# Performance work log

Measured on AMD Instinct MI355X. Metric: run time of the kernel, lower is better.

Reference implementation:

```python
import jax, jax.numpy as jnp
import numpy as np

E, TOPK, H, F, CAP, TP = 8, 2, 1024, 4096, 2048, 1
N = 8192  # tokens * topk (token copies)


def setup_inputs() -> dict:
    key = jax.random.key(0)
    ks = jax.random.split(key, 6)
    inputs_shard = jax.random.normal(ks[0], (N, H), jnp.float32)
    gate_weight = jax.random.uniform(ks[1], (N,), jnp.float32)
    choosed_experts = jax.random.randint(ks[2], (N,), 0, E, dtype=jnp.int32)
    new_index = jax.random.permutation(ks[3], N).astype(jnp.int32)
    w1 = jax.random.normal(ks[4], (E, F, H), jnp.float32) * 0.02
    w2 = jax.random.normal(ks[5], (E, H, F), jnp.float32) * 0.02
    return {"inputs_shard": inputs_shard, "gate_weight": gate_weight,
            "choosed_experts": choosed_experts, "new_index": new_index,
            "w1": w1, "w2": w2}


def _grouped_expert_mlp(x, experts, w1, w2):
    # capacity-based grouped GEMM: sort token copies by expert, pack into
    # (E, CAP, H), run batched fc1->gelu->fc2, unpack back to token order.
    n = x.shape[0]
    order = jnp.argsort(experts)                      # [N]
    se = experts[order]
    offsets = jnp.searchsorted(se, jnp.arange(E))     # start of each expert block
    rank = jnp.arange(n) - offsets[se]                # within-expert position
    valid = rank < CAP                                # CAP=2*N/E, ~never drops
    slot = jnp.where(valid, se * CAP + rank, E * CAP) # out-of-range -> dropped
    buf = jnp.zeros((E * CAP, x.shape[1]), x.dtype).at[slot].set(x[order], mode="drop")
    xe = buf.reshape(E, CAP, -1)                      # [E, CAP, H]
    h = jax.nn.gelu(jnp.einsum("ech,efh->ecf", xe, w1), approximate=False)
    ye = jnp.einsum("ecf,ehf->ech", h, w2).reshape(E * CAP, -1)
    y_sorted = jnp.where(valid[:, None], ye[jnp.clip(slot, 0, E * CAP - 1)], 0.0)
    return jnp.zeros_like(x).at[order].set(y_sorted)  # back to token-copy order


def reference(inputs_shard, gate_weight, choosed_experts, new_index, w1, w2):
    # expert compute, scaled by router probabilities (combine-side scaling)
    result = _grouped_expert_mlp(inputs_shard, choosed_experts, w1, w2)
    result = result * gate_weight[:, None]
    # scatter combine: output1[new_index] = result; full_output += output1
    full_output = jnp.zeros((N, H), result.dtype).at[new_index].set(result)
    # topk reduce: view(N//topk, topk, H).sum(1)
    topk_reduce = full_output.reshape(N // TOPK, TOPK, H).sum(1)
    # reduce_scatter over TP group; TP=1 => identity
    return topk_reduce
```

## Files before the change

kernel.cpp:

```cpp
#include <hip/hip_runtime.h>
#include <stdint.h>

#define N_TOK 8192
#define HDIM  1024
#define FDIM  4096
#define NEXP  8
#define MAXTILES 72

typedef __attribute__((ext_vector_type(8))) __bf16 bf16x8;
typedef __attribute__((ext_vector_type(8))) unsigned short ushort8v;
typedef __attribute__((ext_vector_type(4))) unsigned short ushort4v;
typedef __attribute__((ext_vector_type(4))) float floatx4;

__device__ __forceinline__ unsigned short f2bf(float f) {
  union { float f; uint32_t u; } v; v.f = f;
  uint32_t u = v.u;
  return (unsigned short)((u + 0x7FFFu + ((u >> 16) & 1u)) >> 16);
}

__device__ __forceinline__ void load_lds16(const void* g, void* l) {
  __builtin_amdgcn_global_load_lds(
      (const __attribute__((address_space(1))) void*)(uintptr_t)g,
      (__attribute__((address_space(3))) void*)(uint32_t)(uintptr_t)l,
      16, 0, 0);
}


__global__ void k_count(const int* __restrict__ experts, int* __restrict__ meta) {
  int i = blockIdx.x * 256 + threadIdx.x;
  atomicAdd(&meta[experts[i]], 1);
}

__global__ void k_plan(int* __restrict__ meta) {
  if (threadIdx.x == 0) {
    int off = 0, nt = 0;
    for (int e = 0; e < NEXP; ++e) {
      int c = meta[e];
      meta[8 + e] = off;
      meta[16 + e] = off;
      int t = (c + 127) >> 7;
      for (int k = 0; k < t; ++k) meta[32 + nt++] = (e << 16) | k;
      off += c;
    }
    meta[24] = nt;
  }
}

__global__ void k_scatter(const int* __restrict__ experts, int* __restrict__ meta,
                          int* __restrict__ order) {
  int i = blockIdx.x * 256 + threadIdx.x;
  int e = experts[i];
  int pos = atomicAdd(&meta[16 + e], 1);
  order[pos] = i;
}

__global__ void k_pack(const float* __restrict__ x, const int* __restrict__ order,
                       unsigned short* __restrict__ xs) {
  int s = blockIdx.x;
  int i = order[s];
  int t = threadIdx.x;
  float4 v = *(const float4*)(x + (size_t)i * HDIM + t * 4);
  ushort4v u;
  u[0] = f2bf(v.x); u[1] = f2bf(v.y); u[2] = f2bf(v.z); u[3] = f2bf(v.w);
  *(ushort4v*)(xs + (size_t)s * HDIM + t * 4) = u;
}

__global__ void k_cvt(const float* __restrict__ src, unsigned short* __restrict__ dst) {
  size_t i = ((size_t)blockIdx.x * 256 + threadIdx.x) * 4;
  float4 v = *(const float4*)(src + i);
  ushort4v u;
  u[0] = f2bf(v.x); u[1] = f2bf(v.y); u[2] = f2bf(v.z); u[3] = f2bf(v.w);
  *(ushort4v*)(dst + i) = u;
}

template <bool PRE>
__global__ __launch_bounds__(256) void gemm1_t(
    const unsigned short* __restrict__ xs, const void* __restrict__ w1v,
    unsigned short* __restrict__ h1, const int* __restrict__ meta) {
  __shared__ unsigned short As[128 * 32];
  __shared__ unsigned short Bs[128 * 32];

  int bx = blockIdx.z;
  if (bx >= meta[24]) return;
  int entry = meta[32 + bx];
  int e = entry >> 16, mt = entry & 0xffff;
  int row0 = meta[8 + e] + mt * 128;
  int rend = meta[8 + e] + meta[e];
  int fBase = blockIdx.x * 128;

  int tid = threadIdx.x;
  int w = tid >> 6, lane = tid & 63;
  int r = lane & 15, q = lane >> 4;
  int wm = (w >> 1) * 64, wn = (w & 1) * 64;

  int ar0 = (w * 16) + (lane >> 2);
  int s0 = min(row0 + ar0, N_TOK - 1);
  int s1 = min(row0 + 64 + ar0, N_TOK - 1);
  const unsigned short* ag0 = xs + (size_t)s0 * HDIM + (lane & 3) * 8;
  const unsigned short* ag1 = xs + (size_t)s1 * HDIM + (lane & 3) * 8;
  unsigned short* al0 = &As[(w * 16) * 32];
  unsigned short* al1 = &As[(64 + w * 16) * 32];

  const unsigned short* bg0 = nullptr; const unsigned short* bg1 = nullptr;
  unsigned short* bl0 = nullptr; unsigned short* bl1 = nullptr;
  const float* wbase = nullptr; int brow = 0, bkk = 0;
  if constexpr (PRE) {
    const unsigned short* wb = (const unsigned short*)w1v;
    int br = w * 16 + (lane >> 2);
    bg0 = wb + ((size_t)e * FDIM + fBase + br) * HDIM + (lane & 3) * 8;
    bg1 = bg0 + (size_t)64 * HDIM;
    bl0 = &Bs[(w * 16) * 32];
    bl1 = &Bs[(64 + w * 16) * 32];
  } else {
    brow = tid >> 1; bkk = (tid & 1) * 16;
    wbase = (const float*)w1v + ((size_t)e * FDIM + fBase + brow) * HDIM + bkk;
  }

  floatx4 acc[4][4];
#pragma unroll
  for (int i = 0; i < 4; ++i)
#pragma unroll
    for (int j = 0; j < 4; ++j) acc[i][j] = (floatx4){0.f, 0.f, 0.f, 0.f};

  for (int k0 = 0; k0 < HDIM; k0 += 32) {
    __syncthreads();
    load_lds16(ag0 + k0, al0);
    load_lds16(ag1 + k0, al1);
    if constexpr (PRE) {
      load_lds16(bg0 + k0, bl0);
      load_lds16(bg1 + k0, bl1);
    } else {
      const float* gb = wbase + k0;
      float4 f0 = *(const float4*)(gb);
      float4 f1 = *(const float4*)(gb + 4);
      float4 f2 = *(const float4*)(gb + 8);
      float4 f3 = *(const float4*)(gb + 12);
      ushort8v u0, u1;
      u0[0] = f2bf(f0.x); u0[1] = f2bf(f0.y); u0[2] = f2bf(f0.z); u0[3] = f2bf(f0.w);
      u0[4] = f2bf(f1.x); u0[5] = f2bf(f1.y); u0[6] = f2bf(f1.z); u0[7] = f2bf(f1.w);
      u1[0] = f2bf(f2.x); u1[1] = f2bf(f2.y); u1[2] = f2bf(f2.z); u1[3] = f2bf(f2.w);
      u1[4] = f2bf(f3.x); u1[5] = f2bf(f3.y); u1[6] = f2bf(f3.z); u1[7] = f2bf(f3.w);
      *(ushort8v*)&Bs[brow * 32 + bkk] = u0;
      *(ushort8v*)&Bs[brow * 32 + bkk + 8] = u1;
    }
    __syncthreads();

    bf16x8 av[4], bv[4];
#pragma unroll
    for (int i = 0; i < 4; ++i)
      av[i] = __builtin_bit_cast(bf16x8, *(const ushort8v*)&As[(wm + i * 16 + r) * 32 + q * 8]);
#pragma unroll
    for (int j = 0; j < 4; ++j)
      bv[j] = __builtin_bit_cast(bf16x8, *(const ushort8v*)&Bs[(wn + j * 16 + r) * 32 + q * 8]);
#pragma unroll
    for (int i = 0; i < 4; ++i)
#pragma unroll
      for (int j = 0; j < 4; ++j)
        acc[i][j] = __builtin_amdgcn_mfma_f32_16x16x32_bf16(av[i], bv[j], acc[i][j], 0, 0, 0);
  }

#pragma unroll
  for (int i = 0; i < 4; ++i) {
    int mrow = row0 + wm + i * 16 + q * 4;
#pragma unroll
    for (int reg = 0; reg < 4; ++reg) {
      int s = mrow + reg;
      if (s < rend) {
        unsigned short* dst = h1 + (size_t)s * FDIM + fBase + wn + r;
#pragma unroll
        for (int j = 0; j < 4; ++j) {
          float v = acc[i][j][reg];
          float g = 0.5f * v * (1.0f + erff(v * 0.70710678118654752f));
          dst[j * 16] = f2bf(g);
        }
      }
    }
  }
}

template <bool PRE>
__global__ __launch_bounds__(256) void gemm2_t(
    const unsigned short* __restrict__ h1, const void* __restrict__ w2v,
    const float* __restrict__ gate, const int* __restrict__ new_index,
    float* __restrict__ out, const int* __restrict__ meta) {
  __shared__ unsigned short As[128 * 32];
  __shared__ unsigned short Bs[128 * 32];

  int bx = blockIdx.z;
  if (bx >= meta[24]) return;
  int entry = meta[32 + bx];
  int e = entry >> 16, mt = entry & 0xffff;
  int row0 = meta[8 + e] + mt * 128;
  int rend = meta[8 + e] + meta[e];
  int nBase = blockIdx.x * 128;
  int kStart = blockIdx.y * (FDIM / 2);
  int kEnd = kStart + (FDIM / 2);
  const int* order = meta + 256;

  int tid = threadIdx.x;
  int w = tid >> 6, lane = tid & 63;
  int r = lane & 15, q = lane >> 4;
  int wm = (w >> 1) * 64, wn = (w & 1) * 64;

  int ar0 = (w * 16) + (lane >> 2);
  int s0 = min(row0 + ar0, N_TOK - 1);
  int s1 = min(row0 + 64 + ar0, N_TOK - 1);
  const unsigned short* ag0 = h1 + (size_t)s0 * FDIM + (lane & 3) * 8;
  const unsigned short* ag1 = h1 + (size_t)s1 * FDIM + (lane & 3) * 8;
  unsigned short* al0 = &As[(w * 16) * 32];
  unsigned short* al1 = &As[(64 + w * 16) * 32];

  const unsigned short* bg0 = nullptr; const unsigned short* bg1 = nullptr;
  unsigned short* bl0 = nullptr; unsigned short* bl1 = nullptr;
  const float* wbase = nullptr; int brow = 0, bkk = 0;
  if constexpr (PRE) {
    const unsigned short* wb = (const unsigned short*)w2v;
    int br = w * 16 + (lane >> 2);
    bg0 = wb + ((size_t)e * HDIM + nBase + br) * FDIM + (lane & 3) * 8;
    bg1 = bg0 + (size_t)64 * FDIM;
    bl0 = &Bs[(w * 16) * 32];
    bl1 = &Bs[(64 + w * 16) * 32];
  } else {
    brow = tid >> 1; bkk = (tid & 1) * 16;
    wbase = (const float*)w2v + ((size_t)e * HDIM + nBase + brow) * FDIM + bkk;
  }

  floatx4 acc[4][4];
#pragma unroll
  for (int i = 0; i < 4; ++i)
#pragma unroll
    for (int j = 0; j < 4; ++j) acc[i][j] = (floatx4){0.f, 0.f, 0.f, 0.f};

  for (int k0 = kStart; k0 < kEnd; k0 += 32) {
    __syncthreads();
    load_lds16(ag0 + k0, al0);
    load_lds16(ag1 + k0, al1);
    if constexpr (PRE) {
      load_lds16(bg0 + k0, bl0);
      load_lds16(bg1 + k0, bl1);
    } else {
      const float* gb = wbase + k0;
      float4 f0 = *(const float4*)(gb);
      float4 f1 = *(const float4*)(gb + 4);
      float4 f2 = *(const float4*)(gb + 8);
      float4 f3 = *(const float4*)(gb + 12);
      ushort8v u0, u1;
      u0[0] = f2bf(f0.x); u0[1] = f2bf(f0.y); u0[2] = f2bf(f0.z); u0[3] = f2bf(f0.w);
      u0[4] = f2bf(f1.x); u0[5] = f2bf(f1.y); u0[6] = f2bf(f1.z); u0[7] = f2bf(f1.w);
      u1[0] = f2bf(f2.x); u1[1] = f2bf(f2.y); u1[2] = f2bf(f2.z); u1[3] = f2bf(f2.w);
      u1[4] = f2bf(f3.x); u1[5] = f2bf(f3.y); u1[6] = f2bf(f3.z); u1[7] = f2bf(f3.w);
      *(ushort8v*)&Bs[brow * 32 + bkk] = u0;
      *(ushort8v*)&Bs[brow * 32 + bkk + 8] = u1;
    }
    __syncthreads();

    bf16x8 av[4], bv[4];
#pragma unroll
    for (int i = 0; i < 4; ++i)
      av[i] = __builtin_bit_cast(bf16x8, *(const ushort8v*)&As[(wm + i * 16 + r) * 32 + q * 8]);
#pragma unroll
    for (int j = 0; j < 4; ++j)
      bv[j] = __builtin_bit_cast(bf16x8, *(const ushort8v*)&Bs[(wn + j * 16 + r) * 32 + q * 8]);
#pragma unroll
    for (int i = 0; i < 4; ++i)
#pragma unroll
      for (int j = 0; j < 4; ++j)
        acc[i][j] = __builtin_amdgcn_mfma_f32_16x16x32_bf16(av[i], bv[j], acc[i][j], 0, 0, 0);
  }

#pragma unroll
  for (int i = 0; i < 4; ++i) {
    int mrow = row0 + wm + i * 16 + q * 4;
#pragma unroll
    for (int reg = 0; reg < 4; ++reg) {
      int s = mrow + reg;
      if (s < rend) {
        int itok = order[s];
        float gw = gate[itok];
        int jdx = new_index[itok];
        float* dst = out + (size_t)(jdx >> 1) * HDIM + nBase + wn + r;
#pragma unroll
        for (int j = 0; j < 4; ++j) atomicAdd(dst + j * 16, acc[i][j][reg] * gw);
      }
    }
  }
}

extern "C" void kernel_launch(void* const* d_in, const int* in_sizes, int n_in,
                              void* d_out, int out_size, void* d_ws, size_t ws_size,
                              hipStream_t stream) {
  const float* x        = (const float*)d_in[0];
  const float* gate     = (const float*)d_in[1];
  const int* experts    = (const int*)d_in[2];
  const int* new_index  = (const int*)d_in[3];
  const float* w1       = (const float*)d_in[4];
  const float* w2       = (const float*)d_in[5];
  float* out            = (float*)d_out;

  int* meta = (int*)d_ws;
  int* order = meta + 256;
  const size_t XS_OFF = 65536;
  const size_t XS_SZ  = (size_t)N_TOK * HDIM * 2;
  const size_t H1_SZ  = (size_t)N_TOK * FDIM * 2;
  const size_t W_SZ   = (size_t)NEXP * FDIM * HDIM * 2;
  unsigned short* xs  = (unsigned short*)((char*)d_ws + XS_OFF);
  unsigned short* h1  = (unsigned short*)((char*)d_ws + XS_OFF + XS_SZ);
  unsigned short* w1b = (unsigned short*)((char*)d_ws + XS_OFF + XS_SZ + H1_SZ);
  unsigned short* w2b = (unsigned short*)((char*)d_ws + XS_OFF + XS_SZ + H1_SZ + W_SZ);
  size_t need_small = XS_OFF + XS_SZ + H1_SZ;
  size_t need_big   = need_small + 2 * W_SZ;
  if (ws_size < need_small) return;
  bool big = ws_size >= need_big;

  hipMemsetAsync(d_ws, 0, 4096, stream);
  hipMemsetAsync(d_out, 0, (size_t)out_size * sizeof(float), stream);
  k_count<<<N_TOK / 256, 256, 0, stream>>>(experts, meta);
  k_plan<<<1, 64, 0, stream>>>(meta);
  k_scatter<<<N_TOK / 256, 256, 0, stream>>>(experts, meta, order);
  k_pack<<<N_TOK, 256, 0, stream>>>(x, order, xs);

  if (big) {
    int nblk = (int)((size_t)NEXP * FDIM * HDIM / 4 / 256);
    k_cvt<<<nblk, 256, 0, stream>>>(w1, w1b);
    k_cvt<<<nblk, 256, 0, stream>>>(w2, w2b);
    gemm1_t<true><<<dim3(FDIM / 128, 1, MAXTILES), 256, 0, stream>>>(xs, w1b, h1, meta);
    gemm2_t<true><<<dim3(HDIM / 128, 2, MAXTILES), 256, 0, stream>>>(h1, w2b, gate, new_index, out, meta);
  } else {
    gemm1_t<false><<<dim3(FDIM / 128, 1, MAXTILES), 256, 0, stream>>>(xs, w1, h1, meta);
    gemm2_t<false><<<dim3(HDIM / 128, 2, MAXTILES), 256, 0, stream>>>(h1, w2, gate, new_index, out, meta);
  }
}
```

Measured before the change: 674.7 us.

## Add 256-row tiled double-buffered GEMM kernels with swizzled LDS for bf16 path

Replaces the pre-converted bf16 GEMM path with new 512-thread kernels that use 256x256 (fc1) and 256x128 (fc2) tiles and a K-step of 64. Loads are double-buffered into LDS with explicit vmcnt waits, and the LDS layout is XOR-swizzled to avoid bank conflicts. MFMA issue runs at raised priority. The planner now also emits a 256-row tile list. The larger tiles aim at more operand reuse and overlap of loads with compute, at the cost of higher register/LDS use, occupancy of one block per CU, and more padded rows per expert tile.

```diff
diff --git a/kernel.cpp b/kernel.cpp
--- a/kernel.cpp
+++ b/kernel.cpp
@@ -6,6 +6,7 @@
 #define FDIM  4096
 #define NEXP  8
 #define MAXTILES 72
+#define MAXT256  40
 
 typedef __attribute__((ext_vector_type(8))) __bf16 bf16x8;
 typedef __attribute__((ext_vector_type(8))) unsigned short ushort8v;
@@ -33,16 +34,19 @@
 
 __global__ void k_plan(int* __restrict__ meta) {
   if (threadIdx.x == 0) {
-    int off = 0, nt = 0;
+    int off = 0, nt = 0, nt2 = 0;
     for (int e = 0; e < NEXP; ++e) {
       int c = meta[e];
       meta[8 + e] = off;
       meta[16 + e] = off;
       int t = (c + 127) >> 7;
       for (int k = 0; k < t; ++k) meta[32 + nt++] = (e << 16) | k;
+      int t2 = (c + 255) >> 8;
+      for (int k = 0; k < t2; ++k) meta[104 + nt2++] = (e << 16) | k;
       off += c;
     }
     meta[24] = nt;
+    meta[25] = nt2;
   }
 }
 
@@ -73,6 +77,231 @@
   *(ushort4v*)(dst + i) = u;
 }
 
+
+#define VM_WAIT(n) asm volatile("s_waitcnt vmcnt(" #n ")" ::: "memory")
+
+__global__ __launch_bounds__(512, 1) void gemm1_big(
+    const unsigned short* __restrict__ xs, const unsigned short* __restrict__ wb,
+    unsigned short* __restrict__ h1, const int* __restrict__ meta) {
+  __shared__ unsigned short As[2][256 * 64];
+  __shared__ unsigned short Bs[2][256 * 64];
+
+  int bx = blockIdx.z;
+  if (bx >= meta[25]) return;
+  int entry = meta[104 + bx];
+  int e = entry >> 16, mt = entry & 0xffff;
+  int row0 = meta[8 + e] + mt * 256;
+  int rend = meta[8 + e] + meta[e];
+  int fBase = blockIdx.x * 256;
+
+  int tid = threadIdx.x;
+  int w = tid >> 6, l = tid & 63;
+  int r = l & 15, q = l >> 4;
+
+  int srow = w * 8 + (l >> 3);
+  int scol = ((l & 7) ^ (l >> 3)) << 3;
+  const unsigned short* aP[4];
+  const unsigned short* bP[4];
+#pragma unroll
+  for (int n = 0; n < 4; ++n) {
+    int ar = min(row0 + n * 64 + srow, N_TOK - 1);
+    aP[n] = xs + (size_t)ar * HDIM + scol;
+    int br = fBase + n * 64 + srow;
+    bP[n] = wb + ((size_t)e * FDIM + br) * HDIM + scol;
+  }
+
+  floatx4 acc[8][4];
+#pragma unroll
+  for (int i = 0; i < 8; ++i)
+#pragma unroll
+    for (int j = 0; j < 4; ++j) acc[i][j] = (floatx4){0.f, 0.f, 0.f, 0.f};
+
+  int mb = (w >> 2) * 128;
+  int nb = (w & 3) * 64;
+
+  {
+#pragma unroll
+    for (int n = 0; n < 4; ++n) load_lds16(aP[n], &As[0][n * 4096 + w * 512]);
+#pragma unroll
+    for (int n = 0; n < 4; ++n) load_lds16(bP[n], &Bs[0][n * 4096 + w * 512]);
+  }
+
+  const int NT = HDIM / 64;
+  for (int kt = 0; kt < NT; ++kt) {
+    int cur = kt & 1;
+    if (kt + 1 < NT) {
+      int ko = (kt + 1) * 64;
+      int nxt = cur ^ 1;
+#pragma unroll
+      for (int n = 0; n < 4; ++n) load_lds16(aP[n] + ko, &As[nxt][n * 4096 + w * 512]);
+#pragma unroll
+      for (int n = 0; n < 4; ++n) load_lds16(bP[n] + ko, &Bs[nxt][n * 4096 + w * 512]);
+      VM_WAIT(8);
+    } else {
+      VM_WAIT(0);
+    }
+    __builtin_amdgcn_s_barrier();
+    __builtin_amdgcn_sched_barrier(0);
+
+#pragma unroll
+    for (int kk = 0; kk < 2; ++kk) {
+      bf16x8 av[8], bv[4];
+#pragma unroll
+      for (int i = 0; i < 8; ++i) {
+        int row = mb + i * 16 + r;
+        int col = (kk * 32 + q * 8) ^ ((r & 7) << 3);
+        av[i] = __builtin_bit_cast(bf16x8, *(const ushort8v*)&As[cur][row * 64 + col]);
+      }
+#pragma unroll
+      for (int j = 0; j < 4; ++j) {
+        int row = nb + j * 16 + r;
+        int col = (kk * 32 + q * 8) ^ ((r & 7) << 3);
+        bv[j] = __builtin_bit_cast(bf16x8, *(const ushort8v*)&Bs[cur][row * 64 + col]);
+      }
+      __builtin_amdgcn_s_setprio(1);
+#pragma unroll
+      for (int i = 0; i < 8; ++i)
+#pragma unroll
+        for (int j = 0; j < 4; ++j)
+          acc[i][j] = __builtin_amdgcn_mfma_f32_16x16x32_bf16(av[i], bv[j], acc[i][j], 0, 0, 0);
+      __builtin_amdgcn_s_setprio(0);
+    }
+    __builtin_amdgcn_s_barrier();
+  }
+
+#pragma unroll
+  for (int i = 0; i < 8; ++i) {
+    int mrow = row0 + mb + i * 16 + q * 4;
+#pragma unroll
+    for (int reg = 0; reg < 4; ++reg) {
+      int s = mrow + reg;
+      if (s < rend) {
+        unsigned short* dst = h1 + (size_t)s * FDIM + fBase + nb + r;
+#pragma unroll
+        for (int j = 0; j < 4; ++j) {
+          float v = acc[i][j][reg];
+          float g = 0.5f * v * (1.0f + erff(v * 0.70710678118654752f));
+          dst[j * 16] = f2bf(g);
+        }
+      }
+    }
+  }
+}
+
+__global__ __launch_bounds__(512, 1) void gemm2_big(
+    const unsigned short* __restrict__ h1, const unsigned short* __restrict__ wb,
+    const float* __restrict__ gate, const int* __restrict__ new_index,
+    float* __restrict__ out, const int* __restrict__ meta) {
+  __shared__ unsigned short As[2][256 * 64];
+  __shared__ unsigned short Bs[2][128 * 64];
+
+  int bx = blockIdx.z;
+  if (bx >= meta[25]) return;
+  int entry = meta[104 + bx];
+  int e = entry >> 16, mt = entry & 0xffff;
+  int row0 = meta[8 + e] + mt * 256;
+  int rend = meta[8 + e] + meta[e];
+  int nBase = blockIdx.x * 128;
+  int kStart = blockIdx.y * (FDIM / 2);
+  const int* order = meta + 256;
+
+  int tid = threadIdx.x;
+  int w = tid >> 6, l = tid & 63;
+  int r = l & 15, q = l >> 4;
+
+  int srow = w * 8 + (l >> 3);
+  int scol = ((l & 7) ^ (l >> 3)) << 3;
+  const unsigned short* aP[4];
+  const unsigned short* bP[2];
+#pragma unroll
+  for (int n = 0; n < 4; ++n) {
+    int ar = min(row0 + n * 64 + srow, N_TOK - 1);
+    aP[n] = h1 + (size_t)ar * FDIM + kStart + scol;
+  }
+#pragma unroll
+  for (int n = 0; n < 2; ++n) {
+    int br = nBase + n * 64 + srow;
+    bP[n] = wb + ((size_t)e * HDIM + br) * FDIM + kStart + scol;
+  }
+
+  floatx4 acc[4][4];
+#pragma unroll
+  for (int i = 0; i < 4; ++i)
+#pragma unroll
+    for (int j = 0; j < 4; ++j) acc[i][j] = (floatx4){0.f, 0.f, 0.f, 0.f};
+
+  int mb = (w >> 1) * 64;
+  int nb = (w & 1) * 64;
+
+  {
+#pragma unroll
+    for (int n = 0; n < 4; ++n) load_lds16(aP[n], &As[0][n * 4096 + w * 512]);
+#pragma unroll
+    for (int n = 0; n < 2; ++n) load_lds16(bP[n], &Bs[0][n * 4096 + w * 512]);
+  }
+
+  const int NT = (FDIM / 2) / 64;
+  for (int kt = 0; kt < NT; ++kt) {
+    int cur = kt & 1;
+    if (kt + 1 < NT) {
+      int ko = (kt + 1) * 64;
+      int nxt = cur ^ 1;
+#pragma unroll
+      for (int n = 0; n < 4; ++n) load_lds16(aP[n] + ko, &As[nxt][n * 4096 + w * 512]);
+#pragma unroll
+      for (int n = 0; n < 2; ++n) load_lds16(bP[n] + ko, &Bs[nxt][n * 4096 + w * 512]);
+      VM_WAIT(6);
+    } else {
+      VM_WAIT(0);
+    }
+    __builtin_amdgcn_s_barrier();
+    __builtin_amdgcn_sched_barrier(0);
+
+#pragma unroll
+    for (int kk = 0; kk < 2; ++kk) {
+      bf16x8 av[4], bv[4];
+#pragma unroll
+      for (int i = 0; i < 4; ++i) {
+        int row = mb + i * 16 + r;
+        int col = (kk * 32 + q * 8) ^ ((r & 7) << 3);
+        av[i] = __builtin_bit_cast(bf16x8, *(const ushort8v*)&As[cur][row * 64 + col]);
+      }
+#pragma unroll
+      for (int j = 0; j < 4; ++j) {
+        int row = nb + j * 16 + r;
+        int col = (kk * 32 + q * 8) ^ ((r & 7) << 3);
+        bv[j] = __builtin_bit_cast(bf16x8, *(const ushort8v*)&Bs[cur][row * 64 + col]);
+      }
+      __builtin_amdgcn_s_setprio(1);
+#pragma unroll
+      for (int i = 0; i < 4; ++i)
+#pragma unroll
+        for (int j = 0; j < 4; ++j)
+          acc[i][j] = __builtin_amdgcn_mfma_f32_16x16x32_bf16(av[i], bv[j], acc[i][j], 0, 0, 0);
+      __builtin_amdgcn_s_setprio(0);
+    }
+    __builtin_amdgcn_s_barrier();
+  }
+
+#pragma unroll
+  for (int i = 0; i < 4; ++i) {
+    int mrow = row0 + mb + i * 16 + q * 4;
+#pragma unroll
+    for (int reg = 0; reg < 4; ++reg) {
+      int s = mrow + reg;
+      if (s < rend) {
+        int itok = order[s];
+        float gw = gate[itok];
+        int jdx = new_index[itok];
+        float* dst = out + (size_t)(jdx >> 1) * HDIM + nBase + nb + r;
+#pragma unroll
+        for (int j = 0; j < 4; ++j) atomicAdd(dst + j * 16, acc[i][j][reg] * gw);
+      }
+    }
+  }
+}
+
+
 template <bool PRE>
 __global__ __launch_bounds__(256) void gemm1_t(
     const unsigned short* __restrict__ xs, const void* __restrict__ w1v,
@@ -101,20 +330,9 @@
   unsigned short* al0 = &As[(w * 16) * 32];
   unsigned short* al1 = &As[(64 + w * 16) * 32];
 
-  const unsigned short* bg0 = nullptr; const unsigned short* bg1 = nullptr;
-  unsigned short* bl0 = nullptr; unsigned short* bl1 = nullptr;
   const float* wbase = nullptr; int brow = 0, bkk = 0;
-  if constexpr (PRE) {
-    const unsigned short* wb = (const unsigned short*)w1v;
-    int br = w * 16 + (lane >> 2);
-    bg0 = wb + ((size_t)e * FDIM + fBase + br) * HDIM + (lane & 3) * 8;
-    bg1 = bg0 + (size_t)64 * HDIM;
-    bl0 = &Bs[(w * 16) * 32];
-    bl1 = &Bs[(64 + w * 16) * 32];
-  } else {
-    brow = tid >> 1; bkk = (tid & 1) * 16;
-    wbase = (const float*)w1v + ((size_t)e * FDIM + fBase + brow) * HDIM + bkk;
-  }
+  brow = tid >> 1; bkk = (tid & 1) * 16;
+  wbase = (const float*)w1v + ((size_t)e * FDIM + fBase + brow) * HDIM + bkk;
 
   floatx4 acc[4][4];
 #pragma unroll
@@ -126,10 +344,7 @@
     __syncthreads();
     load_lds16(ag0 + k0, al0);
     load_lds16(ag1 + k0, al1);
-    if constexpr (PRE) {
-      load_lds16(bg0 + k0, bl0);
-      load_lds16(bg1 + k0, bl1);
-    } else {
+    {
       const float* gb = wbase + k0;
       float4 f0 = *(const float4*)(gb);
       float4 f1 = *(const float4*)(gb + 4);
@@ -210,20 +425,9 @@
   unsigned short* al0 = &As[(w * 16) * 32];
   unsigned short* al1 = &As[(64 + w * 16) * 32];
 
-  const unsigned short* bg0 = nullptr; const unsigned short* bg1 = nullptr;
-  unsigned short* bl0 = nullptr; unsigned short* bl1 = nullptr;
   const float* wbase = nullptr; int brow = 0, bkk = 0;
-  if constexpr (PRE) {
-    const unsigned short* wb = (const unsigned short*)w2v;
-    int br = w * 16 + (lane >> 2);
-    bg0 = wb + ((size_t)e * HDIM + nBase + br) * FDIM + (lane & 3) * 8;
-    bg1 = bg0 + (size_t)64 * FDIM;
-    bl0 = &Bs[(w * 16) * 32];
-    bl1 = &Bs[(64 + w * 16) * 32];
-  } else {
-    brow = tid >> 1; bkk = (tid & 1) * 16;
-    wbase = (const float*)w2v + ((size_t)e * HDIM + nBase + brow) * FDIM + bkk;
-  }
+  brow = tid >> 1; bkk = (tid & 1) * 16;
+  wbase = (const float*)w2v + ((size_t)e * HDIM + nBase + brow) * FDIM + bkk;
 
   floatx4 acc[4][4];
 #pragma unroll
@@ -235,10 +439,7 @@
     __syncthreads();
     load_lds16(ag0 + k0, al0);
     load_lds16(ag1 + k0, al1);
-    if constexpr (PRE) {
-      load_lds16(bg0 + k0, bl0);
-      load_lds16(bg1 + k0, bl1);
-    } else {
+    {
       const float* gb = wbase + k0;
       float4 f0 = *(const float4*)(gb);
       float4 f1 = *(const float4*)(gb + 4);
@@ -323,8 +524,8 @@
     int nblk = (int)((size_t)NEXP * FDIM * HDIM / 4 / 256);
     k_cvt<<<nblk, 256, 0, stream>>>(w1, w1b);
     k_cvt<<<nblk, 256, 0, stream>>>(w2, w2b);
-    gemm1_t<true><<<dim3(FDIM / 128, 1, MAXTILES), 256, 0, stream>>>(xs, w1b, h1, meta);
-    gemm2_t<true><<<dim3(HDIM / 128, 2, MAXTILES), 256, 0, stream>>>(h1, w2b, gate, new_index, out, meta);
+    gemm1_big<<<dim3(FDIM / 256, 1, MAXT256), 512, 0, stream>>>(xs, w1b, h1, meta);
+    gemm2_big<<<dim3(HDIM / 128, 2, MAXT256), 512, 0, stream>>>(h1, w2b, gate, new_index, out, meta);
   } else {
     gemm1_t<false><<<dim3(FDIM / 128, 1, MAXTILES), 256, 0, stream>>>(xs, w1, h1, meta);
     gemm2_t<false><<<dim3(HDIM / 128, 2, MAXTILES), 256, 0, stream>>>(h1, w2, gate, new_index, out, meta);
```

Measured after the change: 698.9 us. 1.04x slower.
